# Performance work log

Hardware: AMD Instinct MI355X
Metric: run time of the kernel (lower is better)

The kernel has to match this reference:

```python
import jax, jax.numpy as jnp
import numpy as np

N_STEPS = 100
TAU_S = 5.0  # network_config['tau_s']
SHAPE = (16, 128, 16, 16, N_STEPS)  # [B, C, H, W, T]


def psp(target):
    """Leaky-integrator postsynaptic potential: syn_t = syn_{t-1}*(1-1/tau_s) + x_t, emit syn_t/tau_s."""
    x = jnp.moveaxis(target, -1, 0)  # time-major [T, B, C, H, W]
    decay = 1.0 - 1.0 / TAU_S

    def step(syn, xt):
        syn = syn * decay + xt
        return syn, syn / TAU_S

    _, syns = jax.lax.scan(step, jnp.zeros_like(x[0]), x)
    return jnp.moveaxis(syns, 0, -1)  # back to [B, C, H, W, T]


def setup_inputs() -> dict:
    key = jax.random.key(0)
    k1, k2 = jax.random.split(key)
    outputs = jax.random.normal(k1, SHAPE, dtype=jnp.float32) * 0.1
    target = (jax.random.uniform(k2, SHAPE) < 0.2).astype(jnp.float32)
    return {"outputs": outputs, "target": target}


def reference(outputs, target):
    # SpikeLoss.spike_kernel: 0.5 * sum((outputs - psp(target))**2)
    delta = outputs - psp(target)
    return 0.5 * jnp.sum(delta ** 2)
```

## Files before the change

### kernel.cpp

```cpp
#include <hip/hip_runtime.h>


#define T_STEPS 100
#define N_NEURONS (16 * 128 * 16 * 16)
#define BLOCK 256
#define GRID_P 2048
#define NEUR_PER_WAVE (N_NEURONS / (GRID_P * BLOCK / 64))

__device__ __forceinline__ float wave_scan_psp(float X, int lane) {
  float y;
  y = __shfl_up(X, 1);  if (lane >= 1)  X = fmaf(y, 0.64f, X);
  y = __shfl_up(X, 2);  if (lane >= 2)  X = fmaf(y, 0.4096f, X);
  y = __shfl_up(X, 4);  if (lane >= 4)  X = fmaf(y, 0.16777216f, X);
  y = __shfl_up(X, 8);  if (lane >= 8)  X = fmaf(y, 2.81474977e-2f, X);
  y = __shfl_up(X, 16); if (lane >= 16) X = fmaf(y, 7.92281625e-4f, X);
  y = __shfl_up(X, 32); if (lane >= 32) X = fmaf(y, 6.27710174e-7f, X);
  return X;
}

__global__ __launch_bounds__(BLOCK) void spike_loss_partial(
    const float* __restrict__ outputs,
    const float* __restrict__ target,
    float* __restrict__ partial) {
  const int lane = threadIdx.x & 63;
  const int wave = (blockIdx.x * BLOCK + threadIdx.x) >> 6;
  const bool active = lane < 50;

  float acc = 0.0f;
  size_t n0 = (size_t)wave * NEUR_PER_WAVE;

#pragma unroll 2
  for (int i = 0; i < NEUR_PER_WAVE; ++i) {
    const float* row_t = target + (n0 + i) * T_STEPS;
    const float* row_o = outputs + (n0 + i) * T_STEPS;
    float2 x = active ? reinterpret_cast<const float2*>(row_t)[lane]
                      : make_float2(0.f, 0.f);
    float2 o = active ? reinterpret_cast<const float2*>(row_o)[lane]
                      : make_float2(0.f, 0.f);

    float X = fmaf(x.x, 0.8f, x.y);
    X = wave_scan_psp(X, lane);
    float syn1 = X;
    float syn0 = (X - x.y) * 1.25f;

    float d0 = fmaf(syn0, -0.2f, o.x);
    float d1 = fmaf(syn1, -0.2f, o.y);
    if (active) acc = fmaf(d0, d0, fmaf(d1, d1, acc));
  }

#pragma unroll
  for (int off = 32; off > 0; off >>= 1) acc += __shfl_down(acc, off, 64);

  __shared__ float wsum[BLOCK / 64];
  const int wid = threadIdx.x >> 6;
  if (lane == 0) wsum[wid] = acc;
  __syncthreads();
  if (threadIdx.x == 0)
    partial[blockIdx.x] = wsum[0] + wsum[1] + wsum[2] + wsum[3];
}

__global__ __launch_bounds__(256) void spike_loss_final(
    const float* __restrict__ partial, float* __restrict__ out, int nparts) {
  float acc = 0.0f;
  for (int i = threadIdx.x; i < nparts; i += 256) acc += partial[i];
#pragma unroll
  for (int off = 32; off > 0; off >>= 1) acc += __shfl_down(acc, off, 64);
  __shared__ float wsum[4];
  const int lane = threadIdx.x & 63;
  const int wid = threadIdx.x >> 6;
  if (lane == 0) wsum[wid] = acc;
  __syncthreads();
  if (threadIdx.x == 0) out[0] = 0.5f * (wsum[0] + wsum[1] + wsum[2] + wsum[3]);
}

__global__ __launch_bounds__(BLOCK) void spike_loss_atomic(
    const float* __restrict__ outputs,
    const float* __restrict__ target,
    float* __restrict__ out) {
  const int lane = threadIdx.x & 63;
  const int wave = (blockIdx.x * BLOCK + threadIdx.x) >> 6;
  const bool active = lane < 50;
  float acc = 0.0f;
  size_t n0 = (size_t)wave * NEUR_PER_WAVE;
#pragma unroll 2
  for (int i = 0; i < NEUR_PER_WAVE; ++i) {
    const float* row_t = target + (n0 + i) * T_STEPS;
    const float* row_o = outputs + (n0 + i) * T_STEPS;
    float2 x = active ? reinterpret_cast<const float2*>(row_t)[lane]
                      : make_float2(0.f, 0.f);
    float2 o = active ? reinterpret_cast<const float2*>(row_o)[lane]
                      : make_float2(0.f, 0.f);
    float X = fmaf(x.x, 0.8f, x.y);
    X = wave_scan_psp(X, lane);
    float syn1 = X;
    float syn0 = (X - x.y) * 1.25f;
    float d0 = fmaf(syn0, -0.2f, o.x);
    float d1 = fmaf(syn1, -0.2f, o.y);
    if (active) acc = fmaf(d0, d0, fmaf(d1, d1, acc));
  }
#pragma unroll
  for (int off = 32; off > 0; off >>= 1) acc += __shfl_down(acc, off, 64);
  __shared__ float wsum[BLOCK / 64];
  const int wid = threadIdx.x >> 6;
  if (lane == 0) wsum[wid] = acc;
  __syncthreads();
  if (threadIdx.x == 0)
    atomicAdd(out, 0.5f * (wsum[0] + wsum[1] + wsum[2] + wsum[3]));
}

extern "C" void kernel_launch(void* const* d_in, const int* in_sizes, int n_in,
                              void* d_out, int out_size, void* d_ws, size_t ws_size,
                              hipStream_t stream) {
  const float* outputs = (const float*)d_in[0];
  const float* target = (const float*)d_in[1];
  float* out = (float*)d_out;

  if (ws_size >= GRID_P * sizeof(float)) {
    float* partial = (float*)d_ws;
    spike_loss_partial<<<GRID_P, BLOCK, 0, stream>>>(outputs, target, partial);
    spike_loss_final<<<1, 256, 0, stream>>>(partial, out, GRID_P);
  } else {
    hipMemsetAsync(out, 0, sizeof(float), stream);
    spike_loss_atomic<<<GRID_P, BLOCK, 0, stream>>>(outputs, target, out);
  }
}
```

Before: 414.6 us.

## Process two neurons per wave with float4 loads and a four-step half-wave scan

Each wave now splits into two 32-lane halves, each handling one neuron row. A lane loads a float4 (four timesteps) instead of a float2, so the shuffle scan shrinks from six steps to four and fewer lanes sit idle. The next row's loads are issued one iteration ahead in registers to overlap memory latency with the scan. This raises bandwidth use per instruction and cuts shuffle work, at the cost of more registers and a longer serial recurrence inside each lane for back-solving s0..s2.

```diff
diff --git a/kernel.cpp b/kernel.cpp
--- a/kernel.cpp
+++ b/kernel.cpp
@@ -1,21 +1,71 @@
 #include <hip/hip_runtime.h>
 
 
-#define T_STEPS 100
+#define T4 25
 #define N_NEURONS (16 * 128 * 16 * 16)
 #define BLOCK 256
 #define GRID_P 2048
-#define NEUR_PER_WAVE (N_NEURONS / (GRID_P * BLOCK / 64))
+#define NPW 64
+#define ITERS (NPW / 2)
 
-__device__ __forceinline__ float wave_scan_psp(float X, int lane) {
-  float y;
-  y = __shfl_up(X, 1);  if (lane >= 1)  X = fmaf(y, 0.64f, X);
-  y = __shfl_up(X, 2);  if (lane >= 2)  X = fmaf(y, 0.4096f, X);
-  y = __shfl_up(X, 4);  if (lane >= 4)  X = fmaf(y, 0.16777216f, X);
-  y = __shfl_up(X, 8);  if (lane >= 8)  X = fmaf(y, 2.81474977e-2f, X);
-  y = __shfl_up(X, 16); if (lane >= 16) X = fmaf(y, 7.92281625e-4f, X);
-  y = __shfl_up(X, 32); if (lane >= 32) X = fmaf(y, 6.27710174e-7f, X);
-  return X;
+__device__ __forceinline__ float wave_acc(const float4* __restrict__ t4,
+                                          const float4* __restrict__ o4,
+                                          int wave, int lane) {
+  const int sub = lane & 31;
+  const int half = lane >> 5;
+  const bool active = sub < T4;
+  const int n0 = wave * NPW + half;
+
+  const float4 z = make_float4(0.f, 0.f, 0.f, 0.f);
+  float acc = 0.0f;
+
+  int idx = n0 * T4 + sub;
+  float4 x = active ? t4[idx] : z;
+  float4 o = active ? o4[idx] : z;
+
+  for (int i = 0; i < ITERS; ++i) {
+    float4 xn = z, on = z;
+    if (i + 1 < ITERS) {
+      int idn = (n0 + 2 * (i + 1)) * T4 + sub;
+      if (active) { xn = t4[idn]; on = o4[idn]; }
+    }
+
+    float X = fmaf(fmaf(fmaf(x.x, 0.8f, x.y), 0.8f, x.z), 0.8f, x.w);
+
+    float y;
+    y = __shfl_up(X, 1);  if (sub >= 1) X = fmaf(y, 0.4096f, X);
+    y = __shfl_up(X, 2);  if (sub >= 2) X = fmaf(y, 0.16777216f, X);
+    y = __shfl_up(X, 4);  if (sub >= 4) X = fmaf(y, 2.81474977e-2f, X);
+    y = __shfl_up(X, 8);  if (sub >= 8) X = fmaf(y, 7.92281625e-4f, X);
+
+    float s3 = X;
+    float s2 = (s3 - x.w) * 1.25f;
+    float s1 = (s2 - x.z) * 1.25f;
+    float s0 = (s1 - x.y) * 1.25f;
+
+    float d0 = fmaf(s0, -0.2f, o.x);
+    float d1 = fmaf(s1, -0.2f, o.y);
+    float d2 = fmaf(s2, -0.2f, o.z);
+    float d3 = fmaf(s3, -0.2f, o.w);
+    if (active)
+      acc = fmaf(d0, d0, fmaf(d1, d1, fmaf(d2, d2, fmaf(d3, d3, acc))));
+
+    x = xn; o = on;
+  }
+  return acc;
+}
+
+__device__ __forceinline__ void block_reduce_store(float acc, float* dst,
+                                                   float scale) {
+#pragma unroll
+  for (int off = 32; off > 0; off >>= 1) acc += __shfl_down(acc, off, 64);
+  __shared__ float wsum[BLOCK / 64];
+  const int lane = threadIdx.x & 63;
+  const int wid = threadIdx.x >> 6;
+  if (lane == 0) wsum[wid] = acc;
+  __syncthreads();
+  if (threadIdx.x == 0)
+    dst[0] = scale * (wsum[0] + wsum[1] + wsum[2] + wsum[3]);
 }
 
 __global__ __launch_bounds__(BLOCK) void spike_loss_partial(
@@ -24,39 +74,9 @@
     float* __restrict__ partial) {
   const int lane = threadIdx.x & 63;
   const int wave = (blockIdx.x * BLOCK + threadIdx.x) >> 6;
-  const bool active = lane < 50;
-
-  float acc = 0.0f;
-  size_t n0 = (size_t)wave * NEUR_PER_WAVE;
-
-#pragma unroll 2
-  for (int i = 0; i < NEUR_PER_WAVE; ++i) {
-    const float* row_t = target + (n0 + i) * T_STEPS;
-    const float* row_o = outputs + (n0 + i) * T_STEPS;
-    float2 x = active ? reinterpret_cast<const float2*>(row_t)[lane]
-                      : make_float2(0.f, 0.f);
-    float2 o = active ? reinterpret_cast<const float2*>(row_o)[lane]
-                      : make_float2(0.f, 0.f);
-
-    float X = fmaf(x.x, 0.8f, x.y);
-    X = wave_scan_psp(X, lane);
-    float syn1 = X;
-    float syn0 = (X - x.y) * 1.25f;
-
-    float d0 = fmaf(syn0, -0.2f, o.x);
-    float d1 = fmaf(syn1, -0.2f, o.y);
-    if (active) acc = fmaf(d0, d0, fmaf(d1, d1, acc));
-  }
-
-#pragma unroll
-  for (int off = 32; off > 0; off >>= 1) acc += __shfl_down(acc, off, 64);
-
-  __shared__ float wsum[BLOCK / 64];
-  const int wid = threadIdx.x >> 6;
-  if (lane == 0) wsum[wid] = acc;
-  __syncthreads();
-  if (threadIdx.x == 0)
-    partial[blockIdx.x] = wsum[0] + wsum[1] + wsum[2] + wsum[3];
+  float acc = wave_acc(reinterpret_cast<const float4*>(target),
+                       reinterpret_cast<const float4*>(outputs), wave, lane);
+  block_reduce_store(acc, partial + blockIdx.x, 1.0f);
 }
 
 __global__ __launch_bounds__(256) void spike_loss_final(
@@ -79,25 +99,8 @@
     float* __restrict__ out) {
   const int lane = threadIdx.x & 63;
   const int wave = (blockIdx.x * BLOCK + threadIdx.x) >> 6;
-  const bool active = lane < 50;
-  float acc = 0.0f;
-  size_t n0 = (size_t)wave * NEUR_PER_WAVE;
-#pragma unroll 2
-  for (int i = 0; i < NEUR_PER_WAVE; ++i) {
-    const float* row_t = target + (n0 + i) * T_STEPS;
-    const float* row_o = outputs + (n0 + i) * T_STEPS;
-    float2 x = active ? reinterpret_cast<const float2*>(row_t)[lane]
-                      : make_float2(0.f, 0.f);
-    float2 o = active ? reinterpret_cast<const float2*>(row_o)[lane]
-                      : make_float2(0.f, 0.f);
-    float X = fmaf(x.x, 0.8f, x.y);
-    X = wave_scan_psp(X, lane);
-    float syn1 = X;
-    float syn0 = (X - x.y) * 1.25f;
-    float d0 = fmaf(syn0, -0.2f, o.x);
-    float d1 = fmaf(syn1, -0.2f, o.y);
-    if (active) acc = fmaf(d0, d0, fmaf(d1, d1, acc));
-  }
+  float acc = wave_acc(reinterpret_cast<const float4*>(target),
+                       reinterpret_cast<const float4*>(outputs), wave, lane);
 #pragma unroll
   for (int off = 32; off > 0; off >>= 1) acc += __shfl_down(acc, off, 64);
   __shared__ float wsum[BLOCK / 64];
```

Result: no change. 416.3 us (+0.4%).
